# Kernel tuning notes

Measured on AMD Instinct MI355X. Metric: run time of the kernel, lower is better.

The kernel has to match this reference:

```python
import jax, jax.numpy as jnp
import numpy as np

HEADS = 4
DIM_HEAD = 32


def _ln(x, g, b):
    m = x.mean(-1, keepdims=True)
    v = ((x - m) ** 2).mean(-1, keepdims=True)
    return (x - m) * jax.lax.rsqrt(v + 1e-5) * g + b


def setup_inputs() -> dict:
    key = jax.random.key(0)
    ks = jax.random.split(key, 9)
    b, n, X, Y, W1, W2, d = 4, 6, 10, 10, 10, 10, 128
    x, y, w1, w2 = 10, 10, 4, 4
    inner = HEADS * DIM_HEAD  # 128 == d
    init = 0.02
    return {
        "q": jax.random.normal(ks[0], (b, n, X, Y, W1, W2, d), jnp.float32),
        "k": jax.random.normal(ks[1], (b, n, x, y, w1, w2, d), jnp.float32),
        "v": jax.random.normal(ks[2], (b, n, x, y, w1, w2, d), jnp.float32),
        "skip": jax.random.normal(ks[3], (b, X, Y, W1, W2, d), jnp.float32),
        "head_gate": jax.random.uniform(ks[4], (HEADS,), jnp.float32, 0.5, 1.5),
        "ln_q_g": jnp.ones((d,), jnp.float32), "ln_q_b": jnp.zeros((d,), jnp.float32),
        "ln_k_g": jnp.ones((d,), jnp.float32), "ln_k_b": jnp.zeros((d,), jnp.float32),
        "ln_v_g": jnp.ones((d,), jnp.float32), "ln_v_b": jnp.zeros((d,), jnp.float32),
        "wq": jax.random.normal(ks[5], (d, inner), jnp.float32) * init,
        "bq": jnp.zeros((inner,), jnp.float32),
        "wk": jax.random.normal(ks[6], (d, inner), jnp.float32) * init,
        "bk": jnp.zeros((inner,), jnp.float32),
        "wv": jax.random.normal(ks[7], (d, inner), jnp.float32) * init,
        "bv": jnp.zeros((inner,), jnp.float32),
        "wp": jax.random.normal(ks[8], (inner, d), jnp.float32) * init,
        "bp": jnp.zeros((d,), jnp.float32),
    }


def reference(q, k, v, skip, head_gate,
              ln_q_g, ln_q_b, ln_k_g, ln_k_b, ln_v_g, ln_v_b,
              wq, bq, wk, bk, wv, bv, wp, bp):
    b, n, X, Y, W1, W2, d = q.shape
    _, _, x, y, w1, w2, _ = k.shape
    L = X * Y                      # number of windows (== x*y, asserted in torch)
    Qn = n * W1 * W2               # query tokens per window (views folded in)
    Kn = n * w1 * w2               # kv tokens per window
    # 'b n x y w1 w2 d -> b (x y) (n w1 w2) d'
    qf = q.transpose(0, 2, 3, 1, 4, 5, 6).reshape(b, L, Qn, d)
    kf = k.transpose(0, 2, 3, 1, 4, 5, 6).reshape(b, L, Kn, d)
    vf = v.transpose(0, 2, 3, 1, 4, 5, 6).reshape(b, L, Kn, d)
    # pre-norm + linear qkv projections
    qh = (_ln(qf, ln_q_g, ln_q_b) @ wq + bq).reshape(b, L, Qn, HEADS, DIM_HEAD)
    kh = (_ln(kf, ln_k_g, ln_k_b) @ wk + bk).reshape(b, L, Kn, HEADS, DIM_HEAD)
    vh = (_ln(vf, ln_v_g, ln_v_b) @ wv + bv).reshape(b, L, Kn, HEADS, DIM_HEAD)
    scale = DIM_HEAD ** -0.5
    # windowed attention scores: (b, m, L, Q, K)
    dot = jnp.einsum('blqmd,blkmd->bmlqk', qh * scale, kh)
    dot = dot * head_gate[None, :, None, None, None]  # multiplicative head gate pre-softmax
    att = jax.nn.softmax(dot, axis=-1)
    a = jnp.einsum('bmlqk,blkmd->blqmd', att, vh).reshape(b, L, Qn, HEADS * DIM_HEAD)
    # 'b (x y) (n w1 w2) c -> b n x y w1 w2 c'
    out = a.reshape(b, X, Y, n, W1, W2, HEADS * DIM_HEAD).transpose(0, 3, 1, 2, 4, 5, 6)
    z = out @ wp + bp
    z = z.mean(axis=1)             # mean-pool over views
    return z + skip
```

## Files before the change

kernel.cpp:

```cpp
#include <hip/hip_runtime.h>
#include <hip/hip_bf16.h>

#define DEV __device__ __forceinline__

typedef __attribute__((ext_vector_type(8))) short short8;
typedef __attribute__((ext_vector_type(8))) unsigned short ushort8;
typedef __attribute__((ext_vector_type(4))) float f32x4;
typedef __attribute__((ext_vector_type(2))) unsigned int uint2v;

DEV unsigned short f2bf(float f) {
    unsigned u = __float_as_uint(f);
    unsigned r = u + 0x7fffu + ((u >> 16) & 1u);
    return (unsigned short)(r >> 16);
}
DEV float bf2f(unsigned short h) { return __uint_as_float(((unsigned)h) << 16); }
DEV unsigned cvt_pk_bf16(float lo, float hi) {
    unsigned r;
    asm("v_cvt_pk_bf16_f32 %0, %1, %2" : "=v"(r) : "v"(lo), "v"(hi));
    return r;
}
#define GLDS16(gp, lp)                                                              \
    __builtin_amdgcn_global_load_lds(                                               \
        (const __attribute__((address_space(1))) void*)(gp),                        \
        (__attribute__((address_space(3))) void*)(lp), 16, 0, 0)


__global__ __launch_bounds__(128) void prep_kernel(
    const float* __restrict__ wq, const float* __restrict__ wk,
    const float* __restrict__ wv, const float* __restrict__ wp,
    const float* __restrict__ ln_q_g, const float* __restrict__ ln_q_b,
    const float* __restrict__ ln_k_g, const float* __restrict__ ln_k_b,
    const float* __restrict__ ln_v_g, const float* __restrict__ ln_v_b,
    const float* __restrict__ bq, const float* __restrict__ bk,
    const float* __restrict__ bv, const float* __restrict__ bp,
    const float* __restrict__ head_gate,
    unsigned short* __restrict__ Wt, float* __restrict__ b2)
{
    const int set = blockIdx.x / 9, sub = blockIdx.x % 9;
    const float* W    = set == 0 ? wq : set == 1 ? wk : set == 2 ? wv : wp;
    const float* g    = set == 0 ? ln_q_g : set == 1 ? ln_k_g : ln_v_g;
    const float* e    = set == 0 ? ln_q_b : set == 1 ? ln_k_b : ln_v_b;
    const float* bias = set == 0 ? bq : set == 1 ? bk : set == 2 ? bv : bp;
    const int mode = set == 0 ? 2 : (set == 3 ? 0 : 1);
    const float scale = 0.17677669529663687f;

    if (sub == 0) {
        const int col = threadIdx.x;
        float sg = (mode == 2) ? scale * head_gate[col >> 5] : 1.f;
        float esum = 0.f;
        if (mode >= 1) {
#pragma unroll 8
            for (int k = 0; k < 128; ++k) esum += e[k] * W[k * 128 + col];
        }
        b2[set * 128 + col] = (bias[col] + esum) * sg;
    } else {
        const int k = threadIdx.x;
        const float gk = (mode >= 1) ? g[k] : 1.f;
        const int kk = k >> 5, h = (k >> 3) & 3, j = k & 7;
#pragma unroll
        for (int c = 0; c < 16; ++c) {
            int col = (sub - 1) * 16 + c;
            int nt = col >> 4, q15 = col & 15;
            float sg = (mode == 2) ? scale * head_gate[col >> 5] : 1.f;
            long idx = set * 16384 + (((nt * 4 + kk) * 64 + q15 * 4 + h) << 3) + j;
            Wt[idx] = f2bf(W[k * 128 + col] * gk * sg);
        }
    }
}

__global__ __launch_bounds__(256) void qkv_proj_mfma(
    const float* __restrict__ qsrc, const float* __restrict__ ksrc, const float* __restrict__ vsrc,
    const unsigned short* __restrict__ WtAll, const float* __restrict__ b2All,
    unsigned short* __restrict__ qh, unsigned short* __restrict__ kh, unsigned short* __restrict__ vh)
{
    __shared__ unsigned short WtL[16384];
    __shared__ unsigned short SrcT[4][16 * 132];

    const int bid = blockIdx.x;
    const int tid = threadIdx.x;
    const int w = tid >> 6, lane = tid & 63;
    const int q15 = lane & 15, h = lane >> 4;

    const float* src; unsigned short* dst; int set, isQ, grp;
    if (bid < 4200)      { src = qsrc; dst = qh; set = 0; isQ = 1; grp = bid * 4 + w; }
    else if (bid < 4800) { src = ksrc; dst = kh; set = 1; isQ = 0; grp = (bid - 4200) * 4 + w; }
    else                 { src = vsrc; dst = vh; set = 2; isQ = 0; grp = (bid - 4800) * 4 + w; }
    const unsigned short* WtF = WtAll + set * 16384;
    const float* b2 = b2All + set * 128;

#pragma unroll
    for (int i = 0; i < 8; ++i)
        GLDS16(WtF + i * 2048 + tid * 8, &WtL[i * 2048 + w * 512]);

    long r0; int maxrr;
    if (isQ) {
        int wv6 = grp / 7, t = grp % 7;
        int bl = wv6 / 6, nn = wv6 % 6;
        int b = bl / 100, l = bl % 100;
        r0 = ((long)(b * 6 + nn) * 100 + l) * 100 + t * 16;
        maxrr = (t == 6) ? 3 : 15;
    } else {
        int bl = grp / 6, nn = grp % 6;
        int b = bl / 100, l = bl % 100;
        r0 = ((long)(b * 6 + nn) * 100 + l) * 16;
        maxrr = 15;
    }

    {
        const int half = lane >> 5, li = lane & 31;
        unsigned short* st = SrcT[w];
#pragma unroll
        for (int i = 0; i < 8; ++i) {
            int rr = 2 * i + half;
            int rrc = rr > maxrr ? maxrr : rr;
            f32x4 v = *(const f32x4*)(src + (r0 + rrc) * 128 + li * 4);
            uint2v c;
            c.x = cvt_pk_bf16(v[0], v[1]);
            c.y = cvt_pk_bf16(v[2], v[3]);
            *(uint2v*)&st[rr * 132 + li * 4] = c;
        }
    }

    short8 xr[4];
    float x[4][8];
    {
        const unsigned short* st = SrcT[w];
#pragma unroll
        for (int kk = 0; kk < 4; ++kk) {
            xr[kk] = *(const short8*)&st[q15 * 132 + kk * 32 + h * 8];
#pragma unroll
            for (int j = 0; j < 8; ++j)
                x[kk][j] = bf2f(((unsigned short)xr[kk][j]));
        }
    }

    float s = 0.f, s2 = 0.f;
#pragma unroll
    for (int kk = 0; kk < 4; ++kk)
#pragma unroll
        for (int j = 0; j < 8; ++j) { s += x[kk][j]; s2 += x[kk][j] * x[kk][j]; }
    s  += __shfl_xor(s, 16);  s  += __shfl_xor(s, 32);
    s2 += __shfl_xor(s2, 16); s2 += __shfl_xor(s2, 32);
    const float mean = s * (1.f / 128.f);
    const float var  = s2 * (1.f / 128.f) - mean * mean;
    const float rs  = rsqrtf(var + 1e-5f);
    const float mrs = -mean * rs;

    short8 xf[4];
#pragma unroll
    for (int kk = 0; kk < 4; ++kk) {
        union { unsigned u[4]; short8 s8; } cv;
#pragma unroll
        for (int d = 0; d < 4; ++d)
            cv.u[d] = cvt_pk_bf16(fmaf(x[kk][2 * d], rs, mrs), fmaf(x[kk][2 * d + 1], rs, mrs));
        xf[kk] = cv.s8;
    }

    f32x4 acc[8];
#pragma unroll
    for (int nt = 0; nt < 8; ++nt)
        acc[nt] = *(const f32x4*)(b2 + nt * 16 + h * 4);

    __syncthreads();

#pragma unroll
    for (int kk = 0; kk < 4; ++kk)
#pragma unroll
        for (int nt = 0; nt < 8; ++nt) {
            short8 wf = *(const short8*)&WtL[(((nt * 4 + kk) * 64) + lane) * 8];
            acc[nt] = __builtin_amdgcn_mfma_f32_16x16x32_bf16(wf, xf[kk], acc[nt], 0, 0, 0);
        }

    unsigned short* og = dst + (long)grp * 1024;
#pragma unroll
    for (int nt = 0; nt < 8; ++nt) {
        uint2v pk;
        pk.x = cvt_pk_bf16(acc[nt][0], acc[nt][1]);
        pk.y = cvt_pk_bf16(acc[nt][2], acc[nt][3]);
        *(uint2v*)(og + (nt * 64 + q15 * 4 + h) * 4) = pk;
    }
}

__global__ __launch_bounds__(256, 3) void attn_mfma_kernel(
    const unsigned short* __restrict__ qh, const unsigned short* __restrict__ kh,
    const unsigned short* __restrict__ vh, unsigned short* __restrict__ am)
{
    __shared__ unsigned short Vt[32 * 104];
    __shared__ unsigned short Pt[4][2][16 * 104];

    const int tid = threadIdx.x;
    const int half = blockIdx.x & 1;
    const int m  = (blockIdx.x >> 1) & 3;
    const int bl = blockIdx.x >> 3;
    const int w = tid >> 6, lane = tid & 63;
    const int q15 = lane & 15, h = lane >> 4;
    const int t = half * 4 + w;

    const int coff = (((2 * m + (h >> 1)) * 64) + q15 * 4 + 2 * (h & 1)) * 4;

    short8 kf[6];
#pragma unroll
    for (int ntk = 0; ntk < 6; ++ntk)
        kf[ntk] = *(const short8*)(kh + (long)(bl * 6 + ntk) * 1024 + coff);

    {
        const int d = tid & 31, kt0 = tid >> 5;
        const int f = m * 32 + d;
        const int ntv = f >> 4, hp = (f >> 2) & 3, rg = f & 3;
#pragma unroll
        for (int j = 0; j < 12; ++j) {
            int kt = kt0 + 8 * j;
            Vt[d * 104 + kt] =
                vh[(long)(bl * 6 + (kt >> 4)) * 1024 + ((ntv * 64 + (kt & 15) * 4 + hp) << 2) + rg];
        }
    }
    __syncthreads();

    short8 vf[2][3];
#pragma unroll
    for (int dt = 0; dt < 2; ++dt)
#pragma unroll
        for (int ks = 0; ks < 3; ++ks)
            vf[dt][ks] = *(const short8*)(Vt + (dt * 16 + q15) * 104 + ks * 32 + h * 8);

    if (t >= 7) return;

    const long qgBase = (long)(bl * 6) * 7 * 1024;

    f32x4 o0 = {0.f, 0.f, 0.f, 0.f}, o1 = {0.f, 0.f, 0.f, 0.f};

#pragma unroll
    for (int nn = 0; nn < 6; ++nn) {
        unsigned short* ptw = &Pt[w][nn & 1][0];

        short8 qf = *(const short8*)(qh + qgBase + (long)(nn * 7 + t) * 1024 + coff);

        f32x4 sc[6];
#pragma unroll
        for (int nt = 0; nt < 6; ++nt)
            sc[nt] = __builtin_amdgcn_mfma_f32_16x16x32_bf16(kf[nt], qf, (f32x4){0.f, 0.f, 0.f, 0.f}, 0, 0, 0);

        float p[24];
#pragma unroll
        for (int nt = 0; nt < 6; ++nt)
#pragma unroll
            for (int rg = 0; rg < 4; ++rg)
                p[nt * 4 + rg] = __expf(sc[nt][rg]);

#pragma unroll
        for (int nt = 0; nt < 6; ++nt) {
            uint2v pk;
            pk.x = cvt_pk_bf16(p[nt * 4 + 0], p[nt * 4 + 1]);
            pk.y = cvt_pk_bf16(p[nt * 4 + 2], p[nt * 4 + 3]);
            *(uint2v*)(ptw + q15 * 104 + nt * 16 + h * 4) = pk;
        }

        float s01 = (p[0] + p[1]) + (p[2] + p[3]);
        float s23 = (p[4] + p[5]) + (p[6] + p[7]);
        float s45 = (p[8] + p[9]) + (p[10] + p[11]);
        float s67 = (p[12] + p[13]) + (p[14] + p[15]);
        float s89 = (p[16] + p[17]) + (p[18] + p[19]);
        float sab = (p[20] + p[21]) + (p[22] + p[23]);
        float sum = ((s01 + s23) + (s45 + s67)) + (s89 + sab);
        sum += __shfl_xor(sum, 16);
        sum += __shfl_xor(sum, 32);
        const float inv = __builtin_amdgcn_rcpf(6.f * sum);

        f32x4 t0 = {0.f, 0.f, 0.f, 0.f}, t1 = {0.f, 0.f, 0.f, 0.f};
#pragma unroll
        for (int ks = 0; ks < 3; ++ks) {
            short8 pf = *(const short8*)(ptw + q15 * 104 + ks * 32 + h * 8);
            t0 = __builtin_amdgcn_mfma_f32_16x16x32_bf16(vf[0][ks], pf, t0, 0, 0, 0);
            t1 = __builtin_amdgcn_mfma_f32_16x16x32_bf16(vf[1][ks], pf, t1, 0, 0, 0);
        }

#pragma unroll
        for (int rg = 0; rg < 4; ++rg) {
            o0[rg] += t0[rg] * inv;
            o1[rg] += t1[rg] * inv;
        }
    }

    {
        unsigned short* og = am + (long)(bl * 7 + t) * 1024;
        uint2v a0, a1;
        a0.x = cvt_pk_bf16(o0[0], o0[1]);
        a0.y = cvt_pk_bf16(o0[2], o0[3]);
        a1.x = cvt_pk_bf16(o1[0], o1[1]);
        a1.y = cvt_pk_bf16(o1[2], o1[3]);
        *(uint2v*)(og + ((2 * m) * 64 + q15 * 4 + h) * 4) = a0;
        *(uint2v*)(og + ((2 * m + 1) * 64 + q15 * 4 + h) * 4) = a1;
    }
}

__global__ __launch_bounds__(256) void out_proj_mfma(
    const unsigned short* __restrict__ am, const unsigned short* __restrict__ WtF,
    const float* __restrict__ b2, const float* __restrict__ skip, float* __restrict__ out)
{
    __shared__ unsigned short WtL[16384];

    const int tid = threadIdx.x;
    const int w = tid >> 6, lane = tid & 63;
    const int q15 = lane & 15, h = lane >> 4;
    const int gp = blockIdx.x * 4 + w;
    const int bl = gp / 7, t = gp % 7;
    const int r = t * 16 + q15;
    const long tok = (long)bl * 100 + r;

#pragma unroll
    for (int i = 0; i < 8; ++i)
        GLDS16(WtF + i * 2048 + tid * 8, &WtL[i * 2048 + w * 512]);

    short8 xf[4];
#pragma unroll
    for (int kk = 0; kk < 4; ++kk)
        xf[kk] = *(const short8*)(am + (long)gp * 1024 +
                                  (((2 * kk + (h >> 1)) * 64 + q15 * 4 + 2 * (h & 1)) << 2));

    f32x4 acc[8];
#pragma unroll
    for (int nt = 0; nt < 8; ++nt)
        acc[nt] = *(const f32x4*)(b2 + nt * 16 + h * 4);

    __syncthreads();

#pragma unroll
    for (int kk = 0; kk < 4; ++kk)
#pragma unroll
        for (int nt = 0; nt < 8; ++nt) {
            short8 wf = *(const short8*)&WtL[(((nt * 4 + kk) * 64) + lane) * 8];
            acc[nt] = __builtin_amdgcn_mfma_f32_16x16x32_bf16(wf, xf[kk], acc[nt], 0, 0, 0);
        }

    if (r < 100) {
        const float* srow = skip + tok * 128 + h * 4;
        float* orow = out + tok * 128 + h * 4;
#pragma unroll
        for (int nt = 0; nt < 8; ++nt) {
            f32x4 sk = *(const f32x4*)(srow + nt * 16);
            f32x4 o;
#pragma unroll
            for (int rg = 0; rg < 4; ++rg) o[rg] = acc[nt][rg] + sk[rg];
            *(f32x4*)(orow + nt * 16) = o;
        }
    }
}

extern "C" void kernel_launch(void* const* d_in, const int* in_sizes, int n_in,
                              void* d_out, int out_size, void* d_ws, size_t ws_size,
                              hipStream_t stream) {
    const float* q        = (const float*)d_in[0];
    const float* k        = (const float*)d_in[1];
    const float* v        = (const float*)d_in[2];
    const float* skip     = (const float*)d_in[3];
    const float* head_gate= (const float*)d_in[4];
    const float* ln_q_g   = (const float*)d_in[5];
    const float* ln_q_b   = (const float*)d_in[6];
    const float* ln_k_g   = (const float*)d_in[7];
    const float* ln_k_b   = (const float*)d_in[8];
    const float* ln_v_g   = (const float*)d_in[9];
    const float* ln_v_b   = (const float*)d_in[10];
    const float* wq       = (const float*)d_in[11];
    const float* bq       = (const float*)d_in[12];
    const float* wk       = (const float*)d_in[13];
    const float* bk       = (const float*)d_in[14];
    const float* wv       = (const float*)d_in[15];
    const float* bv       = (const float*)d_in[16];
    const float* wp       = (const float*)d_in[17];
    const float* bp       = (const float*)d_in[18];
    float* out = (float*)d_out;

    char* ws = (char*)d_ws;
    unsigned short* qh = (unsigned short*)(ws);
    unsigned short* kh = (unsigned short*)(ws + 34406400);
    unsigned short* vh = (unsigned short*)(ws + 39321600);
    unsigned short* am = (unsigned short*)(ws + 44236800);
    unsigned short* Wt = (unsigned short*)(ws + 49971200);
    float* b2          = (float*)(ws + 50102272);

    prep_kernel<<<36, 128, 0, stream>>>(wq, wk, wv, wp,
                                        ln_q_g, ln_q_b, ln_k_g, ln_k_b, ln_v_g, ln_v_b,
                                        bq, bk, bv, bp, head_gate, Wt, b2);
    qkv_proj_mfma<<<5400, 256, 0, stream>>>(q, k, v, Wt, b2, qh, kh, vh);
    attn_mfma_kernel<<<3200, 256, 0, stream>>>(qh, kh, vh, am);
    out_proj_mfma<<<700, 256, 0, stream>>>(am, Wt + 3 * 16384, b2 + 3 * 128, skip, out);
}
```

Measured before the change: 87.73 us.

## Make QKV projection persistent over 8 groups per warp with prefetched loads

```diff
diff --git a/kernel.cpp b/kernel.cpp
--- a/kernel.cpp
+++ b/kernel.cpp
@@ -80,11 +80,12 @@
     const int tid = threadIdx.x;
     const int w = tid >> 6, lane = tid & 63;
     const int q15 = lane & 15, h = lane >> 4;
-
-    const float* src; unsigned short* dst; int set, isQ, grp;
-    if (bid < 4200)      { src = qsrc; dst = qh; set = 0; isQ = 1; grp = bid * 4 + w; }
-    else if (bid < 4800) { src = ksrc; dst = kh; set = 1; isQ = 0; grp = (bid - 4200) * 4 + w; }
-    else                 { src = vsrc; dst = vh; set = 2; isQ = 0; grp = (bid - 4800) * 4 + w; }
+    const int hf = lane >> 5, li = lane & 31;
+
+    const float* src; unsigned short* dst; int set, isQ, gbase;
+    if (bid < 525)      { src = qsrc; dst = qh; set = 0; isQ = 1; gbase = bid * 32; }
+    else if (bid < 600) { src = ksrc; dst = kh; set = 1; isQ = 0; gbase = (bid - 525) * 32; }
+    else                { src = vsrc; dst = vh; set = 2; isQ = 0; gbase = (bid - 600) * 32; }
     const unsigned short* WtF = WtAll + set * 16384;
     const float* b2 = b2All + set * 128;
 
@@ -92,92 +93,111 @@
     for (int i = 0; i < 8; ++i)
         GLDS16(WtF + i * 2048 + tid * 8, &WtL[i * 2048 + w * 512]);
 
-    long r0; int maxrr;
-    if (isQ) {
-        int wv6 = grp / 7, t = grp % 7;
-        int bl = wv6 / 6, nn = wv6 % 6;
-        int b = bl / 100, l = bl % 100;
-        r0 = ((long)(b * 6 + nn) * 100 + l) * 100 + t * 16;
-        maxrr = (t == 6) ? 3 : 15;
-    } else {
-        int bl = grp / 6, nn = grp % 6;
-        int b = bl / 100, l = bl % 100;
-        r0 = ((long)(b * 6 + nn) * 100 + l) * 16;
-        maxrr = 15;
-    }
-
-    {
-        const int half = lane >> 5, li = lane & 31;
-        unsigned short* st = SrcT[w];
-#pragma unroll
-        for (int i = 0; i < 8; ++i) {
-            int rr = 2 * i + half;
-            int rrc = rr > maxrr ? maxrr : rr;
-            f32x4 v = *(const f32x4*)(src + (r0 + rrc) * 128 + li * 4);
-            uint2v c;
-            c.x = cvt_pk_bf16(v[0], v[1]);
-            c.y = cvt_pk_bf16(v[2], v[3]);
-            *(uint2v*)&st[rr * 132 + li * 4] = c;
-        }
-    }
-
-    short8 xr[4];
-    float x[4][8];
-    {
-        const unsigned short* st = SrcT[w];
+    auto rowPtr = [&](int grp, int rr) -> const float* {
+        long r0; int maxrr;
+        if (isQ) {
+            int wv6 = grp / 7, t = grp % 7;
+            int bl = wv6 / 6, nn = wv6 % 6;
+            int b = bl / 100, l = bl % 100;
+            r0 = ((long)(b * 6 + nn) * 100 + l) * 100 + t * 16;
+            maxrr = (t == 6) ? 3 : 15;
+        } else {
+            int bl = grp / 6, nn = grp % 6;
+            int b = bl / 100, l = bl % 100;
+            r0 = ((long)(b * 6 + nn) * 100 + l) * 16;
+            maxrr = 15;
+        }
+        int rrc = rr > maxrr ? maxrr : rr;
+        return src + (r0 + rrc) * 128 + li * 4;
+    };
+
+    f32x4 xs[8];
+#pragma unroll
+    for (int j = 0; j < 8; ++j)
+        xs[j] = *(const f32x4*)rowPtr(gbase + w, 2 * j + hf);
+
+    __syncthreads();
+
+#pragma unroll
+    for (int i = 0; i < 8; ++i) {
+        const int grp = gbase + i * 4 + w;
+
+        uint2v c16[8];
+#pragma unroll
+        for (int j = 0; j < 8; ++j) {
+            c16[j].x = cvt_pk_bf16(xs[j][0], xs[j][1]);
+            c16[j].y = cvt_pk_bf16(xs[j][2], xs[j][3]);
+        }
+
+        if (i < 7) {
+#pragma unroll
+            for (int j = 0; j < 8; ++j)
+                xs[j] = *(const f32x4*)rowPtr(gbase + (i + 1) * 4 + w, 2 * j + hf);
+        }
+
+        {
+            unsigned short* st = SrcT[w];
+#pragma unroll
+            for (int j = 0; j < 8; ++j)
+                *(uint2v*)&st[(2 * j + hf) * 132 + li * 4] = c16[j];
+        }
+
+        short8 xr[4];
+        float x[4][8];
+        {
+            const unsigned short* st = SrcT[w];
+#pragma unroll
+            for (int kk = 0; kk < 4; ++kk) {
+                xr[kk] = *(const short8*)&st[q15 * 132 + kk * 32 + h * 8];
+#pragma unroll
+                for (int j = 0; j < 8; ++j)
+                    x[kk][j] = bf2f(((unsigned short)xr[kk][j]));
+            }
+        }
+
+        float s = 0.f, s2 = 0.f;
+#pragma unroll
+        for (int kk = 0; kk < 4; ++kk)
+#pragma unroll
+            for (int j = 0; j < 8; ++j) { s += x[kk][j]; s2 += x[kk][j] * x[kk][j]; }
+        s  += __shfl_xor(s, 16);  s  += __shfl_xor(s, 32);
+        s2 += __shfl_xor(s2, 16); s2 += __shfl_xor(s2, 32);
+        const float mean = s * (1.f / 128.f);
+        const float var  = s2 * (1.f / 128.f) - mean * mean;
+        const float rs  = rsqrtf(var + 1e-5f);
+        const float mrs = -mean * rs;
+
+        short8 xf[4];
 #pragma unroll
         for (int kk = 0; kk < 4; ++kk) {
-            xr[kk] = *(const short8*)&st[q15 * 132 + kk * 32 + h * 8];
-#pragma unroll
-            for (int j = 0; j < 8; ++j)
-                x[kk][j] = bf2f(((unsigned short)xr[kk][j]));
-        }
-    }
-
-    float s = 0.f, s2 = 0.f;
-#pragma unroll
-    for (int kk = 0; kk < 4; ++kk)
-#pragma unroll
-        for (int j = 0; j < 8; ++j) { s += x[kk][j]; s2 += x[kk][j] * x[kk][j]; }
-    s  += __shfl_xor(s, 16);  s  += __shfl_xor(s, 32);
-    s2 += __shfl_xor(s2, 16); s2 += __shfl_xor(s2, 32);
-    const float mean = s * (1.f / 128.f);
-    const float var  = s2 * (1.f / 128.f) - mean * mean;
-    const float rs  = rsqrtf(var + 1e-5f);
-    const float mrs = -mean * rs;
-
-    short8 xf[4];
-#pragma unroll
-    for (int kk = 0; kk < 4; ++kk) {
-        union { unsigned u[4]; short8 s8; } cv;
-#pragma unroll
-        for (int d = 0; d < 4; ++d)
-            cv.u[d] = cvt_pk_bf16(fmaf(x[kk][2 * d], rs, mrs), fmaf(x[kk][2 * d + 1], rs, mrs));
-        xf[kk] = cv.s8;
-    }
-
-    f32x4 acc[8];
-#pragma unroll
-    for (int nt = 0; nt < 8; ++nt)
-        acc[nt] = *(const f32x4*)(b2 + nt * 16 + h * 4);
-
-    __syncthreads();
-
-#pragma unroll
-    for (int kk = 0; kk < 4; ++kk)
+            union { unsigned u[4]; short8 s8; } cv;
+#pragma unroll
+            for (int d = 0; d < 4; ++d)
+                cv.u[d] = cvt_pk_bf16(fmaf(x[kk][2 * d], rs, mrs), fmaf(x[kk][2 * d + 1], rs, mrs));
+            xf[kk] = cv.s8;
+        }
+
+        f32x4 acc[8];
+#pragma unroll
+        for (int nt = 0; nt < 8; ++nt)
+            acc[nt] = *(const f32x4*)(b2 + nt * 16 + h * 4);
+
+#pragma unroll
+        for (int kk = 0; kk < 4; ++kk)
+#pragma unroll
+            for (int nt = 0; nt < 8; ++nt) {
+                short8 wf = *(const short8*)&WtL[(((nt * 4 + kk) * 64) + lane) * 8];
+                acc[nt] = __builtin_amdgcn_mfma_f32_16x16x32_bf16(wf, xf[kk], acc[nt], 0, 0, 0);
+            }
+
+        unsigned short* og = dst + (long)grp * 1024;
 #pragma unroll
         for (int nt = 0; nt < 8; ++nt) {
-            short8 wf = *(const short8*)&WtL[(((nt * 4 + kk) * 64) + lane) * 8];
-            acc[nt] = __builtin_amdgcn_mfma_f32_16x16x32_bf16(wf, xf[kk], acc[nt], 0, 0, 0);
-        }
-
-    unsigned short* og = dst + (long)grp * 1024;
-#pragma unroll
-    for (int nt = 0; nt < 8; ++nt) {
-        uint2v pk;
-        pk.x = cvt_pk_bf16(acc[nt][0], acc[nt][1]);
-        pk.y = cvt_pk_bf16(acc[nt][2], acc[nt][3]);
-        *(uint2v*)(og + (nt * 64 + q15 * 4 + h) * 4) = pk;
+            uint2v pk;
+            pk.x = cvt_pk_bf16(acc[nt][0], acc[nt][1]);
+            pk.y = cvt_pk_bf16(acc[nt][2], acc[nt][3]);
+            *(uint2v*)(og + (nt * 64 + q15 * 4 + h) * 4) = pk;
+        }
     }
 }
 
@@ -381,7 +401,7 @@
     prep_kernel<<<36, 128, 0, stream>>>(wq, wk, wv, wp,
                                         ln_q_g, ln_q_b, ln_k_g, ln_k_b, ln_v_g, ln_v_b,
                                         bq, bk, bv, bp, head_gate, Wt, b2);
-    qkv_proj_mfma<<<5400, 256, 0, stream>>>(q, k, v, Wt, b2, qh, kh, vh);
+    qkv_proj_mfma<<<675, 256, 0, stream>>>(q, k, v, Wt, b2, qh, kh, vh);
     attn_mfma_kernel<<<3200, 256, 0, stream>>>(qh, kh, vh, am);
     out_proj_mfma<<<700, 256, 0, stream>>>(am, Wt + 3 * 16384, b2 + 3 * 128, skip, out);
 }
```

Measured after the change: 89.12 us. No clear change (+1.6%).
